# Kernel optimization log

Measured on AMD Instinct MI355X. Metric: run time of the kernel, lower is better.

## Reference

```python
import jax, jax.numpy as jnp
import numpy as np

N_SITES = 16
BATCH = 8192
K = 256
EPS = 1e-10


def _entanglement_entropy(sites_A, sites_B):
    # sites_A: [b, pA, k], sites_B: [b, pB, k]
    corr = jnp.einsum('bik,bjk->bij', sites_A, sites_B)  # [b, pA, pB]
    s = jnp.linalg.svd(corr, compute_uv=False)           # [b, min(pA,pB)]
    s_sq = s * s + EPS
    p = s_sq / jnp.sum(s_sq, axis=-1, keepdims=True)
    return -jnp.sum(p * jnp.log(p + EPS), axis=-1)        # [b]


def setup_inputs() -> dict:
    key = jax.random.key(0)
    sites = jax.random.normal(key, (BATCH, N_SITES, K), dtype=jnp.float32)
    return {"sites": sites}


def reference(sites) -> jnp.ndarray:
    # sites: [batch, n_sites, k]; list-of-tensors in the original, stacked here.
    n = sites.shape[1]
    mid = n // 2  # 8
    # Whole-system bipartition
    S_whole = _entanglement_entropy(sites[:, :mid], sites[:, mid:])
    # Left half bipartition (mid_left = mid // 2 = 4)
    ml = mid // 2
    S_left = _entanglement_entropy(sites[:, :ml], sites[:, ml:mid])
    # Right half bipartition
    nr = n - mid
    mr = nr // 2
    S_right = _entanglement_entropy(sites[:, mid:mid + mr], sites[:, mid + mr:])
    phi_q = S_whole - (S_left + S_right)
    return jax.nn.relu(phi_q)
```

## Files before the change

kernel.cpp:

```cpp
#include <hip/hip_runtime.h>
#include <math.h>

#define DEV __device__ __forceinline__

DEV float rcp_fast(float x) { return __builtin_amdgcn_rcpf(x); }
DEV float rsq_fast(float x) { return __builtin_amdgcn_rsqf(x); }

__host__ __device__ constexpr int TI(int n, int i, int j) {
  return n * i - (i * (i - 1)) / 2 + (j - i);
}

template <int N>
DEV float& sym_at(float (&a)[N * (N + 1) / 2], int i, int j) {
  return (i <= j) ? a[TI(N, i, j)] : a[TI(N, j, i)];
}

template <int N>
DEV void pivot_params(float (&a)[N * (N + 1) / 2], int p, int q,
                      float& c_out, float& s_out) {
  float apq = a[TI(N, p, q)];
  float app = a[TI(N, p, p)];
  float aqq = a[TI(N, q, q)];
  float h = aqq - app;
  float tw = apq + apq;
  float den = fabsf(h) + sqrtf(fmaf(h, h, tw * tw)) + 1e-37f;
  float t = tw * rcp_fast(den);
  t = (h < 0.0f) ? -t : t;
  float c = rsq_fast(fmaf(t, t, 1.0f));
  float s = t * c;
  c_out = c;
  s_out = s;
  a[TI(N, p, p)] = fmaf(-t, apq, app);
  a[TI(N, q, q)] = fmaf( t, apq, aqq);
  a[TI(N, p, q)] = 0.0f;
}

template <int N>
DEV void cross_update(float (&a)[N * (N + 1) / 2], int pa, int qa, int pb,
                      int qb, float ca, float sa, float cb, float sb) {
  float w = sym_at<N>(a, pa, pb), x = sym_at<N>(a, pa, qb);
  float y = sym_at<N>(a, qa, pb), z = sym_at<N>(a, qa, qb);
  float w1 = fmaf(ca, w, -sa * y), x1 = fmaf(ca, x, -sa * z);
  float y1 = fmaf(sa, w,  ca * y), z1 = fmaf(sa, x,  ca * z);
  sym_at<N>(a, pa, pb) = fmaf(cb, w1, -sb * x1);
  sym_at<N>(a, pa, qb) = fmaf(sb, w1,  cb * x1);
  sym_at<N>(a, qa, pb) = fmaf(cb, y1, -sb * z1);
  sym_at<N>(a, qa, qb) = fmaf(sb, y1,  cb * z1);
}

template <int SWEEPS>
DEV void pjacobi8(float (&a)[36]) {
  constexpr int P[7][4][2] = {
      {{0, 7}, {1, 6}, {2, 5}, {3, 4}}, {{0, 1}, {2, 7}, {3, 6}, {4, 5}},
      {{0, 2}, {1, 3}, {4, 7}, {5, 6}}, {{0, 3}, {2, 4}, {1, 5}, {6, 7}},
      {{0, 4}, {3, 5}, {2, 6}, {1, 7}}, {{0, 5}, {4, 6}, {3, 7}, {1, 2}},
      {{0, 6}, {5, 7}, {1, 4}, {2, 3}}};
  for (int sw = 0; sw < SWEEPS; ++sw) {
#pragma unroll
    for (int r = 0; r < 7; ++r) {
      float cc[4], ss[4];
#pragma unroll
      for (int u = 0; u < 4; ++u)
        pivot_params<8>(a, P[r][u][0], P[r][u][1], cc[u], ss[u]);
#pragma unroll
      for (int u = 0; u < 4; ++u) {
#pragma unroll
        for (int v = u + 1; v < 4; ++v) {
          cross_update<8>(a, P[r][u][0], P[r][u][1], P[r][v][0], P[r][v][1],
                          cc[u], ss[u], cc[v], ss[v]);
        }
      }
    }
  }
}

template <int SWEEPS>
DEV void pjacobi4x2(float (&a)[10], float (&b)[10]) {
  constexpr int P[3][2][2] = {
      {{0, 3}, {1, 2}}, {{0, 1}, {2, 3}}, {{0, 2}, {1, 3}}};
  for (int sw = 0; sw < SWEEPS; ++sw) {
#pragma unroll
    for (int r = 0; r < 3; ++r) {
      float ca0, sa0, ca1, sa1, cb0, sb0, cb1, sb1;
      pivot_params<4>(a, P[r][0][0], P[r][0][1], ca0, sa0);
      pivot_params<4>(b, P[r][0][0], P[r][0][1], cb0, sb0);
      pivot_params<4>(a, P[r][1][0], P[r][1][1], ca1, sa1);
      pivot_params<4>(b, P[r][1][0], P[r][1][1], cb1, sb1);
      cross_update<4>(a, P[r][0][0], P[r][0][1], P[r][1][0], P[r][1][1], ca0,
                      sa0, ca1, sa1);
      cross_update<4>(b, P[r][0][0], P[r][0][1], P[r][1][0], P[r][1][1], cb0,
                      sb0, cb1, sb1);
    }
  }
}

template <int N>
DEV float entropy_of(const float (&a)[N * (N + 1) / 2]) {
  float lam[N];
  float sum = 0.0f;
#pragma unroll
  for (int i = 0; i < N; ++i) {
    float l = fmaxf(a[TI(N, i, i)], 0.0f) + 1e-10f;
    lam[i] = l;
    sum += l;
  }
  float inv = 1.0f / sum;
  float H = 0.0f;
#pragma unroll
  for (int i = 0; i < N; ++i) {
    float p = lam[i] * inv;
    H = fmaf(p, __logf(p + 1e-10f), H);
  }
  return -H;
}

DEV float reduce_dist_64(float (&cur)[64], int lane) {
#pragma unroll
  for (int d = 0; d < 6; ++d) {
    const int dist = 1 << d;
    const int up = (lane >> d) & 1;
#pragma unroll
    for (int m = 0; m < (64 >> (d + 1)); ++m) {
      float snd = up ? cur[2 * m]     : cur[2 * m + 1];
      float kp  = up ? cur[2 * m + 1] : cur[2 * m];
      float r = __shfl_xor(snd, dist, 64);
      cur[m] = kp + r;
    }
  }
  return cur[0];
}

DEV float reduce_dist_32(float (&cur)[32], int lane) {
#pragma unroll
  for (int d = 0; d < 5; ++d) {
    const int dist = 1 << d;
    const int up = (lane >> d) & 1;
#pragma unroll
    for (int m = 0; m < (32 >> (d + 1)); ++m) {
      float snd = up ? cur[2 * m]     : cur[2 * m + 1];
      float kp  = up ? cur[2 * m + 1] : cur[2 * m];
      float r = __shfl_xor(snd, dist, 64);
      cur[m] = kp + r;
    }
  }
  float v = cur[0];
  v += __shfl_xor(v, 32, 64);
  return v;
}

__global__ __launch_bounds__(64) void corr_kernel(
    const float* __restrict__ sites, float* __restrict__ cmat) {
  const int b = blockIdx.x;
  const int lane = threadIdx.x;
  const float4* base = reinterpret_cast<const float4*>(sites) + (size_t)b * 1024;

  float4 v[16];
#pragma unroll
  for (int s = 0; s < 16; ++s) v[s] = base[s * 64 + lane];

  float aw[64];
#pragma unroll
  for (int i = 0; i < 8; ++i) {
#pragma unroll
    for (int j = 0; j < 8; ++j) {
      float4 a = v[i], c = v[8 + j];
      aw[i * 8 + j] =
          fmaf(a.x, c.x, fmaf(a.y, c.y, fmaf(a.z, c.z, a.w * c.w)));
    }
  }
  float cw = reduce_dist_64(aw, lane);

  float alr[32];
#pragma unroll
  for (int i = 0; i < 4; ++i) {
#pragma unroll
    for (int j = 0; j < 4; ++j) {
      float4 a = v[i], c = v[4 + j];
      alr[i * 4 + j] =
          fmaf(a.x, c.x, fmaf(a.y, c.y, fmaf(a.z, c.z, a.w * c.w)));
      float4 a2 = v[8 + i], c2 = v[12 + j];
      alr[16 + i * 4 + j] =
          fmaf(a2.x, c2.x, fmaf(a2.y, c2.y, fmaf(a2.z, c2.z, a2.w * c2.w)));
    }
  }
  float clr = reduce_dist_32(alr, lane);

  cmat[(size_t)lane * 8192 + b] = cw;
  if (lane < 32) cmat[(size_t)(64 + lane) * 8192 + b] = clr;
}

__global__ __launch_bounds__(64) void phi_kernel(
    const float* __restrict__ cmat, float* __restrict__ out) {
  const int b = blockIdx.x * 64 + threadIdx.x;

  float Cw[64];
#pragma unroll
  for (int e = 0; e < 64; ++e) Cw[e] = cmat[(size_t)e * 8192 + b];
  float Mw[36];
#pragma unroll
  for (int i = 0; i < 8; ++i) {
#pragma unroll
    for (int j = i; j < 8; ++j) {
      float acc = 0.0f;
#pragma unroll
      for (int k = 0; k < 8; ++k) acc = fmaf(Cw[i * 8 + k], Cw[j * 8 + k], acc);
      Mw[TI(8, i, j)] = acc;
    }
  }

  float Cl[16], Cr[16];
#pragma unroll
  for (int e = 0; e < 16; ++e) Cl[e] = cmat[(size_t)(64 + e) * 8192 + b];
#pragma unroll
  for (int e = 0; e < 16; ++e) Cr[e] = cmat[(size_t)(80 + e) * 8192 + b];
  float Ml[10], Mr[10];
#pragma unroll
  for (int i = 0; i < 4; ++i) {
#pragma unroll
    for (int j = i; j < 4; ++j) {
      float accl = 0.0f, accr = 0.0f;
#pragma unroll
      for (int k = 0; k < 4; ++k) {
        accl = fmaf(Cl[i * 4 + k], Cl[j * 4 + k], accl);
        accr = fmaf(Cr[i * 4 + k], Cr[j * 4 + k], accr);
      }
      Ml[TI(4, i, j)] = accl;
      Mr[TI(4, i, j)] = accr;
    }
  }

  pjacobi8<5>(Mw);
  pjacobi4x2<4>(Ml, Mr);

  float Sw = entropy_of<8>(Mw);
  float Sl = entropy_of<4>(Ml);
  float Sr = entropy_of<4>(Mr);

  out[b] = fmaxf(Sw - Sl - Sr, 0.0f);
}

extern "C" void kernel_launch(void* const* d_in, const int* in_sizes, int n_in,
                              void* d_out, int out_size, void* d_ws, size_t ws_size,
                              hipStream_t stream) {
  const float* sites = (const float*)d_in[0];
  float* out = (float*)d_out;
  float* cmat = (float*)d_ws;

  corr_kernel<<<8192, 64, 0, stream>>>(sites, cmat);
  phi_kernel<<<128, 64, 0, stream>>>(cmat, out);
}
```

Measured before the change: 212.9 us.

## Store correlations row-major per batch, stage via LDS, and cut Jacobi sweeps

The correlation kernel now writes each batch's 96 values contiguously, so its stores no longer scatter with an 8192-element stride. The phi kernel loads a 64-batch tile with coalesced float4 reads into padded shared memory and each thread reads its own row back from there. Separately, the Jacobi sweep counts drop from 5 to 4 (8x8) and from 4 to 3 (4x4 pair), which cuts ALU work but risks eigenvalues converging less accurately.

```diff
diff --git a/kernel.cpp b/kernel.cpp
--- a/kernel.cpp
+++ b/kernel.cpp
@@ -185,17 +185,43 @@
   }
   float clr = reduce_dist_32(alr, lane);
 
-  cmat[(size_t)lane * 8192 + b] = cw;
-  if (lane < 32) cmat[(size_t)(64 + lane) * 8192 + b] = clr;
+  float* row = cmat + (size_t)b * 96;
+  row[lane] = cw;
+  if (lane < 32) row[64 + lane] = clr;
 }
 
 __global__ __launch_bounds__(64) void phi_kernel(
     const float* __restrict__ cmat, float* __restrict__ out) {
-  const int b = blockIdx.x * 64 + threadIdx.x;
-
-  float Cw[64];
-#pragma unroll
-  for (int e = 0; e < 64; ++e) Cw[e] = cmat[(size_t)e * 8192 + b];
+  __shared__ float4 lds[64 * 25];
+  const int t = threadIdx.x;
+  const int b0 = blockIdx.x * 64;
+
+  const float4* src = reinterpret_cast<const float4*>(cmat) + (size_t)b0 * 24;
+#pragma unroll
+  for (int r = 0; r < 24; ++r) {
+    int q = r * 64 + t;
+    float4 val = src[q];
+    int bl = q / 24;
+    int e4 = q - bl * 24;
+    lds[bl * 25 + e4] = val;
+  }
+  __syncthreads();
+
+  const float4* myrow = &lds[t * 25];
+  float Cw[64], Cl[16], Cr[16];
+#pragma unroll
+  for (int j = 0; j < 16; ++j) {
+    float4 f = myrow[j];
+    Cw[4 * j] = f.x; Cw[4 * j + 1] = f.y; Cw[4 * j + 2] = f.z; Cw[4 * j + 3] = f.w;
+  }
+#pragma unroll
+  for (int j = 0; j < 4; ++j) {
+    float4 f = myrow[16 + j];
+    Cl[4 * j] = f.x; Cl[4 * j + 1] = f.y; Cl[4 * j + 2] = f.z; Cl[4 * j + 3] = f.w;
+    float4 g = myrow[20 + j];
+    Cr[4 * j] = g.x; Cr[4 * j + 1] = g.y; Cr[4 * j + 2] = g.z; Cr[4 * j + 3] = g.w;
+  }
+
   float Mw[36];
 #pragma unroll
   for (int i = 0; i < 8; ++i) {
@@ -207,12 +233,6 @@
       Mw[TI(8, i, j)] = acc;
     }
   }
-
-  float Cl[16], Cr[16];
-#pragma unroll
-  for (int e = 0; e < 16; ++e) Cl[e] = cmat[(size_t)(64 + e) * 8192 + b];
-#pragma unroll
-  for (int e = 0; e < 16; ++e) Cr[e] = cmat[(size_t)(80 + e) * 8192 + b];
   float Ml[10], Mr[10];
 #pragma unroll
   for (int i = 0; i < 4; ++i) {
@@ -229,14 +249,14 @@
     }
   }
 
-  pjacobi8<5>(Mw);
-  pjacobi4x2<4>(Ml, Mr);
+  pjacobi8<4>(Mw);
+  pjacobi4x2<3>(Ml, Mr);
 
   float Sw = entropy_of<8>(Mw);
   float Sl = entropy_of<4>(Ml);
   float Sr = entropy_of<4>(Mr);
 
-  out[b] = fmaxf(Sw - Sl - Sr, 0.0f);
+  out[b0 + t] = fmaxf(Sw - Sl - Sr, 0.0f);
 }
 
 extern "C" void kernel_launch(void* const* d_in, const int* in_sizes, int n_in,
```

Measured after the change: 203.5 us. 1.05x faster.
